# Kernel optimization log

Measured on AMD Instinct MI355X. Metric: run time of the kernel, lower is better.

## Reference

```python
import jax, jax.numpy as jnp
import numpy as np

MIN_HAIRPIN = 4
BIG = 1e30  # stand-in for the numpy reference's 1e18 INF (fp32-safe)


def _dp_single(e_pair, e_unp, allowed):
    """Nussinov min-energy DP for one sequence.
    e_pair: (L,L) f32, e_unp: (L,) f32, allowed: (L,L) bool.
    Returns dp (L,L) and ptr (L,L) backpointers matching the numpy reference:
      0 -> i unpaired, 1 -> j unpaired, 2 -> (i,j) paired, k+3 -> bifurcation at k.
    Vectorised over the antidiagonal (all i for a fixed span s at once).
    """
    L = e_unp.shape[0]
    idx = jnp.arange(L)
    dp0 = jnp.full((L, L), BIG, dtype=e_pair.dtype).at[idx, idx].set(e_unp)
    ptr0 = jnp.full((L, L), -1, dtype=jnp.int32).at[idx, idx].set(0)
    t = jnp.arange(L - 1)  # bifurcation offset k = i + t

    def step(carry, s):
        dp, ptr = carry
        j = idx + s - 1
        valid = j < L
        jc = jnp.minimum(j, L - 1)
        ip1 = jnp.minimum(idx + 1, L - 1)
        jm1 = jnp.maximum(jc - 1, 0)
        opt0 = dp[ip1, jc] + e_unp            # i unpaired
        opt1 = dp[idx, jm1] + e_unp[jc]       # j unpaired
        inner = jnp.where(s >= 3, dp[ip1, jm1], 0.0)
        pair_ok = allowed[idx, jc] & (s - 1 > MIN_HAIRPIN)  # j - i = s - 1
        opt2 = jnp.where(pair_ok, inner + e_pair[idx, jc], BIG)
        k = jnp.minimum(idx[:, None] + t[None, :], L - 1)
        bif = dp[idx[:, None], k] + dp[jnp.minimum(k + 1, L - 1), jc[:, None]]
        bif = jnp.where(t[None, :] < s - 1, bif, BIG)
        cand = jnp.concatenate([opt0[:, None], opt1[:, None], opt2[:, None], bif], axis=1)
        c = jnp.argmin(cand, axis=1)  # first-occurrence argmin == strict-< tie-break
        best = jnp.take_along_axis(cand, c[:, None], axis=1)[:, 0]
        new_ptr = jnp.where(c < 3, c, c + idx).astype(jnp.int32)  # c-3 is offset t -> k+3 = c+i
        dp = dp.at[idx, jc].set(jnp.where(valid, best, dp[idx, jc]))
        ptr = ptr.at[idx, jc].set(jnp.where(valid, new_ptr, ptr[idx, jc]))
        return (dp, ptr), None

    (dp, ptr), _ = jax.lax.scan(step, (dp0, ptr0), jnp.arange(2, L + 1))
    return dp, ptr


def _traceback(ptr):
    """Stack-based traceback of the backpointer matrix. Returns pairs (L,) int32, -1 = unpaired."""
    L = ptr.shape[0]

    def cond(st):
        return st[2] > 0

    def body(st):
        si, sj, sp, res = st
        top = sp - 1
        i, j = si[top], sj[top]
        skip = i >= j
        p = ptr[i, j]
        is0, is1, is2, isk = p == 0, p == 1, p == 2, p >= 3
        k = p - 3
        p1i = jnp.where(is0 | is2, i + 1, i)
        p1j = jnp.where(is1 | is2, j - 1, jnp.where(isk, k, j))
        v1 = (~skip) & jnp.where(is2, i + 1 <= j - 1, True)
        v2 = (~skip) & isk  # bifurcation pushes a second interval (k+1, j)
        res = jnp.where(is2 & (~skip), res.at[i].set(j).at[j].set(i), res)
        si = si.at[top].set(jnp.where(v1, p1i, si[top]))
        sj = sj.at[top].set(jnp.where(v1, p1j, sj[top]))
        slot2 = top + v1.astype(jnp.int32)
        si = si.at[slot2].set(jnp.where(v2, k + 1, si[slot2]))
        sj = sj.at[slot2].set(jnp.where(v2, j, sj[slot2]))
        sp = top + v1.astype(jnp.int32) + v2.astype(jnp.int32)
        return si, sj, sp, res

    si0 = jnp.zeros((L,), jnp.int32)
    sj0 = jnp.zeros((L,), jnp.int32).at[0].set(L - 1)
    res0 = jnp.full((L,), -1, jnp.int32)
    _, _, _, res = jax.lax.while_loop(cond, body, (si0, sj0, jnp.int32(1), res0))
    return res


def _structure_energy(e_pair, e_unp, pairs):
    """E(x,S) = sum_{i unpaired} e_unp[i] + sum_{(i,j) in S, i<j} e_pair[i,j]."""
    L = e_unp.shape[-1]
    clamped = jnp.maximum(pairs, 0)
    unp = jnp.where(pairs < 0, e_unp, 0.0).sum(-1)
    pe = jnp.take_along_axis(e_pair, clamped[..., None], axis=2)[..., 0]
    is_pair = (pairs >= 0) & (jnp.arange(L)[None, :] < clamped)
    return unp + jnp.where(is_pair, pe, 0.0).sum(-1)


def setup_inputs() -> dict:
    key = jax.random.key(0)
    k1, k2, k3 = jax.random.split(key, 3)
    B, L = 32, 384
    e_pair = jax.random.normal(k1, (B, L, L), jnp.float32)
    e_unp = jax.random.normal(k2, (B, L), jnp.float32)
    pair_mask = jax.random.randint(k3, (B, L, L), 0, 2).astype(jnp.bool_)
    return {"e_pair": e_pair, "e_unp": e_unp, "pair_mask": pair_mask}


def reference(e_pair, e_unp, pair_mask):
    dp, ptr = jax.vmap(_dp_single)(e_pair, e_unp, pair_mask)
    pairs = jax.vmap(_traceback)(ptr)  # (B, L) int32, -1 = unpaired
    energy = _structure_energy(e_pair, e_unp, pairs)  # (B,), equals dp[:, 0, -1]
    return pairs, energy
```

## Files before the change

### kernel.cpp

```cpp
#include <hip/hip_runtime.h>

#define LSEQ 384
#define BATCH 32
#define BIGV 1e30f
#define TB_STK 448
#define NN ((size_t)LSEQ * LSEQ)
#define BT 32
#define NT 12
#define PIT 33

__device__ __forceinline__ int detect_mmode_wave(const unsigned char* m0, int lane) {
    unsigned char v = m0[lane & 63];
    unsigned long long big = __ballot(v >= 2);
    unsigned long long off = __ballot((((lane & 63) & 3) != 0) && (v != 0));
    return big ? 2 : (off ? 1 : 0);
}
__device__ __forceinline__ bool mask_read(const void* mask, size_t idx, int mmode) {
    if (mmode == 0) return ((const unsigned int*)mask)[idx] != 0;
    if (mmode == 1) return ((const unsigned char*)mask)[idx] != 0;
    return ((const unsigned short*)mask)[idx] != 0;
}
__device__ __forceinline__ void choice_write(void* mask, size_t idx, int c, int mmode) {
    if (mmode == 0) ((unsigned int*)mask)[idx] = (unsigned int)c;
    else if (mmode == 1) ((unsigned char*)mask)[idx] = (unsigned char)c;
    else ((unsigned short*)mask)[idx] = (unsigned short)c;
}

__device__ __forceinline__ float edge_min32(const float* rowp, const float* colp) {
    float a0 = BIGV, a1 = BIGV, a2 = BIGV, a3 = BIGV;
    #pragma unroll
    for (int kk = 0; kk < 32; kk += 4) {
        float r0 = rowp[kk], r1 = rowp[kk + 1], r2 = rowp[kk + 2], r3 = rowp[kk + 3];
        const float* cb = colp + kk * PIT;
        float c0 = cb[0], c1 = cb[PIT], c2 = cb[2 * PIT], c3 = cb[3 * PIT];
        a0 = fminf(a0, r0 + c0); a1 = fminf(a1, r1 + c1);
        a2 = fminf(a2, r2 + c2); a3 = fminf(a3, r3 + c3);
    }
    return fminf(fminf(a0, a1), fminf(a2, a3));
}

__device__ __forceinline__ void minplus_waves(
    const float* __restrict__ dpG, int I, int J, const int* fm, int nfm,
    int wv, int lane, float part[4][BT][PIT])
{
    const int r0 = (lane >> 3) << 2, c0 = (lane & 7) << 2;
    float r16[16];
    #pragma unroll
    for (int z = 0; z < 16; ++z) r16[z] = BIGV;
    const int mi = wv >> 1, kqB = (wv & 1) * 4;
    if (mi < nfm) {
        const int M = fm[mi];
        #pragma unroll
        for (int q = 0; q < 4; ++q) {
            const int k = M * BT + (kqB + q) * 4;
            float4 a0 = *(const float4*)&dpG[(size_t)(I * BT + r0 + 0) * LSEQ + k];
            float4 a1 = *(const float4*)&dpG[(size_t)(I * BT + r0 + 1) * LSEQ + k];
            float4 a2 = *(const float4*)&dpG[(size_t)(I * BT + r0 + 2) * LSEQ + k];
            float4 a3 = *(const float4*)&dpG[(size_t)(I * BT + r0 + 3) * LSEQ + k];
            float4 b0 = *(const float4*)&dpG[(size_t)(J * BT + c0 + 0) * LSEQ + k];
            float4 b1 = *(const float4*)&dpG[(size_t)(J * BT + c0 + 1) * LSEQ + k];
            float4 b2 = *(const float4*)&dpG[(size_t)(J * BT + c0 + 2) * LSEQ + k];
            float4 b3 = *(const float4*)&dpG[(size_t)(J * BT + c0 + 3) * LSEQ + k];
            #pragma unroll
            for (int ri = 0; ri < 4; ++ri) {
                float4 av = ri == 0 ? a0 : ri == 1 ? a1 : ri == 2 ? a2 : a3;
                #pragma unroll
                for (int ci = 0; ci < 4; ++ci) {
                    float4 bv = ci == 0 ? b0 : ci == 1 ? b1 : ci == 2 ? b2 : b3;
                    float m = fminf(fminf(av.x + bv.x, av.y + bv.y),
                                    fminf(av.z + bv.z, av.w + bv.w));
                    r16[ri * 4 + ci] = fminf(r16[ri * 4 + ci], m);
                }
            }
        }
    }
    #pragma unroll
    for (int ri = 0; ri < 4; ++ri)
        #pragma unroll
        for (int ci = 0; ci < 4; ++ci)
            part[wv][r0 + ri][c0 + ci] = r16[ri * 4 + ci];
}

__device__ __constant__ int c_sb4[12] = {0,0,0,0, 0, 8, 15, 21, 26, 30, 33, 35};

__global__ __launch_bounds__(64) void diag_kernel(
    float* __restrict__ e_pair, const float* __restrict__ e_unp, void* mask)
{
    __shared__ float dT[BT + 1][PIT];
    __shared__ float epm[BT][PIT];
    __shared__ float s_eunp[BT];

    const int bid = blockIdx.x;
    const int b = bid / NT, t = bid % NT;
    const int lane = threadIdx.x;
    float* dpG = e_pair + (size_t)b * NN;
    const size_t mb = (size_t)b * NN;
    const int mmode = detect_mmode_wave((const unsigned char*)mask, lane);

    for (int z = lane; z < (BT + 1) * PIT; z += 64) ((float*)dT)[z] = BIGV;
    __syncthreads();
    if (lane < BT) {
        int i = t * BT + lane;
        float v = e_unp[b * LSEQ + i];
        s_eunp[lane] = v;
        dT[lane][lane] = v;
        dpG[(size_t)i * LSEQ + i] = v;
        if (i > 0) dpG[(size_t)i * LSEQ + i - 1] = v;
    }
    for (int z = lane; z < BT * BT; z += 64) {
        int li = z >> 5, lj = z & 31;
        int i = t * BT + li, j = t * BT + lj;
        bool ok = (lj - li > 4) && mask_read(mask, mb + (size_t)i * LSEQ + j, mmode);
        epm[li][lj] = ok ? dpG[(size_t)i * LSEQ + j] : BIGV;
    }
    __syncthreads();

    const int idx = lane >> 1, h = lane & 1;
    for (int sg = 1; sg < BT; ++sg) {
        const int nc = BT - sg;
        const bool act = idx < nc;
        const int li = idx, lj = idx + sg;
        const int ljc = lj < BT ? lj : BT - 1;
        const int i = t * BT + li, j = t * BT + lj;
        float ev = edge_min32(&dT[li][0], &dT[1][ljc]);
        float e1 = BIGV, opt0 = 0.f, x1 = BIGV, x2 = BIGV;
        if (act) {
            if (h == 0) {
                e1 = ev;
                opt0 = dT[li + 1][lj] + s_eunp[li];
            } else {
                x1 = dT[li][lj - 1] + s_eunp[lj];
                float pe = epm[li][lj];
                if (pe < BIGV) x2 = dT[li + 1][lj - 1] + pe;
            }
        }
        float y1 = __shfl_xor(x1, 1), y2 = __shfl_xor(x2, 1);
        if (act && h == 0) {
            float best = fminf(e1, y2);
            int cch = (best == opt0) ? 0 : (best == y1) ? 1
                     : (best == y2 && y2 < BIGV) ? 2 : 3;
            dT[li][lj] = best;
            dpG[(size_t)i * LSEQ + j] = best;
            if (i > 0) dpG[(size_t)j * LSEQ + i - 1] = best;
            choice_write(mask, mb + (size_t)j * LSEQ + i, cch, mmode);
        }
    }
}

__global__ __launch_bounds__(256) void step_kernel(
    float* __restrict__ e_pair, const float* __restrict__ e_unp,
    void* mask, float* __restrict__ acc, int p)
{
    __shared__ float dTI[BT + 1][PIT], dTJ[BT + 1][PIT];
    __shared__ float cur[BT + 1][PIT];
    __shared__ float epm[BT][PIT];
    __shared__ float part[4][BT][PIT];
    __shared__ float brow[BT], bcol[BT], s_eI[BT], s_eJ[BT];
    __shared__ float bcorn;

    const int b = blockIdx.x % BATCH;
    const int u = blockIdx.x / BATCH;
    const int nswp = NT - p;
    const int tid = threadIdx.x, lane = tid & 63, wv = tid >> 6;
    float* dpG = e_pair + (size_t)b * NN;
    const size_t mb = (size_t)b * NN;

    if (u >= nswp) {
        int e = u - nswp, s2 = p + 1;
        while (s2 < NT && e >= NT - s2) { e -= NT - s2; ++s2; }
        const int I = e, J = I + s2;
        int fm[2]; fm[0] = I + p - 1; int nfm = 1;
        if (J - (p - 1) != fm[0]) fm[nfm++] = J - (p - 1);
        minplus_waves(dpG, I, J, fm, nfm, wv, lane, part);
        __syncthreads();
        float* accT = acc + ((size_t)(b * 36 + c_sb4[s2] + I) << 10);
        const bool first = (p == (s2 + 1) / 2 + 1);
        for (int z = tid; z < BT * BT; z += 256) {
            int li = z >> 5, lj = z & 31;
            float m = fminf(fminf(part[0][li][lj], part[1][li][lj]),
                            fminf(part[2][li][lj], part[3][li][lj]));
            accT[z] = first ? m : fminf(accT[z], m);
        }
        return;
    }

    const int I = u, J = I + p, s = p;
    const int mmode = detect_mmode_wave((const unsigned char*)mask, lane);

    for (int z = tid; z < BT * BT; z += 256) {
        int li = z >> 5, lj = z & 31;
        dTI[li][lj] = (lj >= li) ? dpG[(size_t)(I * BT + li) * LSEQ + I * BT + lj] : BIGV;
        dTJ[li][lj] = (lj >= li) ? dpG[(size_t)(J * BT + li) * LSEQ + J * BT + lj] : BIGV;
    }
    for (int z = tid; z < PIT; z += 256) {
        dTI[BT][z] = BIGV; dTJ[BT][z] = BIGV; cur[BT][z] = BIGV;
    }
    if (tid < BT) {
        brow[tid] = dpG[(size_t)((I + 1) * BT) * LSEQ + J * BT + tid];
        s_eI[tid] = e_unp[b * LSEQ + I * BT + tid];
    } else if (tid < 2 * BT) {
        int q = tid - BT;
        bcol[q] = dpG[(size_t)(I * BT + q) * LSEQ + J * BT - 1];
        s_eJ[q] = e_unp[b * LSEQ + J * BT + q];
    } else if (tid == 2 * BT) {
        bcorn = (s >= 2) ? dpG[(size_t)((I + 1) * BT) * LSEQ + J * BT - 1] : BIGV;
    }
    for (int z = tid; z < BT * BT; z += 256) {
        int li = z >> 5, lj = z & 31;
        int i = I * BT + li, j = J * BT + lj;
        bool ok = (j - i > 4) && mask_read(mask, mb + (size_t)i * LSEQ + j, mmode);
        epm[li][lj] = ok ? dpG[(size_t)i * LSEQ + j] : BIGV;
    }

    int fm[2]; int nfm = 0;
    if (s >= 2) fm[nfm++] = I + 1;
    if (s >= 3) fm[nfm++] = J - 1;
    minplus_waves(dpG, I, J, fm, nfm, wv, lane, part);
    __syncthreads();

    const float* accT = acc + ((size_t)(b * 36 + c_sb4[s] + I) << 10);
    for (int z = tid; z < BT * BT; z += 256) {
        int li = z >> 5, lj = z & 31;
        float m = fminf(fminf(part[0][li][lj], part[1][li][lj]),
                        fminf(part[2][li][lj], part[3][li][lj]));
        if (s >= 4) m = fminf(m, accT[z]);
        cur[li][lj] = m;
    }
    __syncthreads();
    if (wv != 0) return;

    const int idx = lane >> 1, h = lane & 1;
    for (int sg = -(BT - 1); sg <= BT - 1; ++sg) {
        const int asg = sg < 0 ? -sg : sg;
        const int nc = BT - asg;
        const bool act = idx < nc;
        const int li = (sg >= 0) ? idx : idx - sg;
        const int lj = li + sg;
        const int lic = li < BT ? li : BT - 1;
        const int ljc = (lj < BT ? (lj >= 0 ? lj : 0) : BT - 1);
        const int i = I * BT + li, j = J * BT + lj;
        const float* rowp = (h == 0) ? &dTI[lic][0] : &cur[lic][0];
        const float* colp = (h == 0) ? &cur[1][ljc] : &dTJ[1][ljc];
        float ev = edge_min32(rowp, colp);
        float e1 = BIGV, opt0 = 0.f, farv = BIGV;
        float x0 = BIGV, x1 = BIGV, x2 = BIGV;
        if (act) {
            if (h == 0) {
                e1 = fminf(ev, dTI[li][BT - 1] + brow[lj]);
                opt0 = ((li + 1 < BT) ? cur[li + 1][lj] : brow[lj]) + s_eI[li];
                farv = cur[li][lj];
            } else {
                x0 = ev;
                x1 = ((lj >= 1) ? cur[li][lj - 1] : bcol[li]) + s_eJ[lj];
                float pe = epm[li][lj];
                if (pe < BIGV) {
                    float inner = (li + 1 < BT)
                        ? ((lj >= 1) ? cur[li + 1][lj - 1] : bcol[li + 1])
                        : ((lj >= 1) ? brow[lj - 1] : bcorn);
                    x2 = inner + pe;
                }
            }
        }
        float y0 = __shfl_xor(x0, 1), y1 = __shfl_xor(x1, 1), y2 = __shfl_xor(x2, 1);
        if (act && h == 0) {
            float best = fminf(fminf(fminf(e1, y0), farv), y2);
            int cch = (best == opt0) ? 0 : (best == y1) ? 1
                     : (best == y2 && y2 < BIGV) ? 2 : 3;
            cur[li][lj] = best;
            dpG[(size_t)i * LSEQ + j] = best;
            if (i > 0) dpG[(size_t)j * LSEQ + i - 1] = best;
            choice_write(mask, mb + (size_t)j * LSEQ + i, cch, mmode);
        }
    }
}

__global__ __launch_bounds__(512) void tb_kernel(
    const float* __restrict__ e_pair, const void* mask, float* __restrict__ out)
{
    const int b = blockIdx.x;
    const int tid = threadIdx.x;
    const int lane = tid & 63, wv = tid >> 6;
    const float* dp = e_pair + (size_t)b * NN;
    const size_t mb = (size_t)b * NN;
    const int mmode = detect_mmode_wave((const unsigned char*)mask, lane);

    __shared__ __align__(16) unsigned char ch[LSEQ * LSEQ];
    __shared__ short res[LSEQ];
    __shared__ int st[TB_STK];

    if (mmode == 1) {
        const uint4* src = (const uint4*)((const unsigned char*)mask + mb);
        for (int z = tid; z < (int)(NN / 16); z += 512) ((uint4*)ch)[z] = src[z];
    } else if (mmode == 2) {
        const uint4* src = (const uint4*)((const unsigned char*)mask + mb * 2);
        for (int z = tid; z < (int)(NN / 8); z += 512) {
            uint4 v = src[z];
            unsigned int lo = (v.x & 0xFFu) | (((v.x >> 16) & 0xFFu) << 8)
                            | ((v.y & 0xFFu) << 16) | (((v.y >> 16) & 0xFFu) << 24);
            unsigned int hi = (v.z & 0xFFu) | (((v.z >> 16) & 0xFFu) << 8)
                            | ((v.w & 0xFFu) << 16) | (((v.w >> 16) & 0xFFu) << 24);
            ((unsigned int*)ch)[z * 2] = lo;
            ((unsigned int*)ch)[z * 2 + 1] = hi;
        }
    } else {
        const uint4* src = (const uint4*)((const unsigned char*)mask + mb * 4);
        for (int z = tid; z < (int)(NN / 4); z += 512) {
            uint4 v = src[z];
            ((unsigned int*)ch)[z] = (v.x & 0xFFu) | ((v.y & 0xFFu) << 8)
                                   | ((v.z & 0xFFu) << 16) | ((v.w & 0xFFu) << 24);
        }
    }
    for (int l = tid; l < LSEQ; l += 512) res[l] = -1;
    __syncthreads();
    if (wv != 0) return;

    int sp = 0;
    int ci = 0, cj = LSEQ - 1;
    int have = 1;
    for (int iter = 0; iter < 8192; ++iter) {
        if (!have) {
            if (sp == 0) break;
            --sp;
            int pk = st[sp];
            ci = pk >> 16; cj = pk & 0xFFFF;
        }
        have = 0;
        if (ci >= cj) continue;
        int c = ch[(size_t)cj * LSEQ + ci];
        if (c == 0) { ++ci; have = 1; }
        else if (c == 1) { --cj; have = 1; }
        else if (c == 2) {
            res[ci] = (short)cj; res[cj] = (short)ci;
            if (ci + 1 <= cj - 1) { ++ci; --cj; have = 1; }
        } else {
            const int d = cj - ci;
            const float* rowi = dp + (size_t)ci * LSEQ;
            const float* mrow = dp + (size_t)cj * LSEQ;
            float bv = BIGV; int bt = d;
            for (int t = lane; t < d; t += 64) {
                float cc = rowi[ci + t] + mrow[ci + t];
                if (cc < bv || (cc == bv && t < bt)) { bv = cc; bt = t; }
            }
            for (int m = 32; m > 0; m >>= 1) {
                float ov = __shfl_xor(bv, m, 64);
                int   ot = __shfl_xor(bt, m, 64);
                if (ov < bv || (ov == bv && ot < bt)) { bv = ov; bt = ot; }
            }
            int k = ci + bt;
            if (sp < TB_STK - 1) { st[sp] = ((k + 1) << 16) | cj; ++sp; }
            cj = k; have = 1;
        }
    }

    for (int l = lane; l < LSEQ; l += 64)
        out[b * LSEQ + l] = (float)res[l];
    if (lane == 0)
        out[BATCH * LSEQ + b] = dp[LSEQ - 1];
}

extern "C" void kernel_launch(void* const* d_in, const int* in_sizes, int n_in,
                              void* d_out, int out_size, void* d_ws, size_t ws_size,
                              hipStream_t stream) {
    float* e_pair = (float*)d_in[0];
    const float* e_unp = (const float*)d_in[1];
    void* mask = d_in[2];
    float* acc = (float*)d_ws;
    (void)ws_size;

    static const int updC[12] = {0, 0, 0, 8, 13, 15, 14, 10, 6, 3, 1, 0};

    diag_kernel<<<BATCH * NT, 64, 0, stream>>>(e_pair, e_unp, mask);
    for (int p = 1; p < NT; ++p)
        step_kernel<<<BATCH * (NT - p + updC[p]), 256, 0, stream>>>(
            e_pair, e_unp, mask, acc, p);
    tb_kernel<<<BATCH, 512, 0, stream>>>(e_pair, mask, (float*)d_out);
}
```

Measured before the change: 775.6 us.

## Fuse diagonal and wavefront step kernels into one cooperative persistent kernel

Replaces the diag kernel and the eleven per-wavefront step kernel launches with a single cooperative kernel. It loops over tiles with a grid-stride loop and uses grid.sync() between wavefront phases. This removes per-launch overhead and the gaps between kernel boundaries. In exchange, the diagonal phase now runs in 256-thread blocks with only one wave active, the grid is capped by occupancy, and every phase pays a grid-wide barrier.

```diff
diff --git a/kernel.cpp b/kernel.cpp
--- a/kernel.cpp
+++ b/kernel.cpp
@@ -1,4 +1,5 @@
 #include <hip/hip_runtime.h>
+#include <hip/hip_cooperative_groups.h>
 
 #define LSEQ 384
 #define BATCH 32
@@ -8,6 +9,8 @@
 #define BT 32
 #define NT 12
 #define PIT 33
+
+namespace cg = cooperative_groups;
 
 __device__ __forceinline__ int detect_mmode_wave(const unsigned char* m0, int lane) {
     unsigned char v = m0[lane & 63];
@@ -82,75 +85,14 @@
 }
 
 __device__ __constant__ int c_sb4[12] = {0,0,0,0, 0, 8, 15, 21, 26, 30, 33, 35};
-
-__global__ __launch_bounds__(64) void diag_kernel(
-    float* __restrict__ e_pair, const float* __restrict__ e_unp, void* mask)
+__device__ __constant__ int c_updC[12] = {0, 0, 0, 8, 13, 15, 14, 10, 6, 3, 1, 0};
+
+__global__ __launch_bounds__(256, 3) void dp_coop(
+    float* __restrict__ e_pair, const float* __restrict__ e_unp,
+    void* mask, float* __restrict__ acc)
 {
-    __shared__ float dT[BT + 1][PIT];
-    __shared__ float epm[BT][PIT];
-    __shared__ float s_eunp[BT];
-
-    const int bid = blockIdx.x;
-    const int b = bid / NT, t = bid % NT;
-    const int lane = threadIdx.x;
-    float* dpG = e_pair + (size_t)b * NN;
-    const size_t mb = (size_t)b * NN;
-    const int mmode = detect_mmode_wave((const unsigned char*)mask, lane);
-
-    for (int z = lane; z < (BT + 1) * PIT; z += 64) ((float*)dT)[z] = BIGV;
-    __syncthreads();
-    if (lane < BT) {
-        int i = t * BT + lane;
-        float v = e_unp[b * LSEQ + i];
-        s_eunp[lane] = v;
-        dT[lane][lane] = v;
-        dpG[(size_t)i * LSEQ + i] = v;
-        if (i > 0) dpG[(size_t)i * LSEQ + i - 1] = v;
-    }
-    for (int z = lane; z < BT * BT; z += 64) {
-        int li = z >> 5, lj = z & 31;
-        int i = t * BT + li, j = t * BT + lj;
-        bool ok = (lj - li > 4) && mask_read(mask, mb + (size_t)i * LSEQ + j, mmode);
-        epm[li][lj] = ok ? dpG[(size_t)i * LSEQ + j] : BIGV;
-    }
-    __syncthreads();
-
-    const int idx = lane >> 1, h = lane & 1;
-    for (int sg = 1; sg < BT; ++sg) {
-        const int nc = BT - sg;
-        const bool act = idx < nc;
-        const int li = idx, lj = idx + sg;
-        const int ljc = lj < BT ? lj : BT - 1;
-        const int i = t * BT + li, j = t * BT + lj;
-        float ev = edge_min32(&dT[li][0], &dT[1][ljc]);
-        float e1 = BIGV, opt0 = 0.f, x1 = BIGV, x2 = BIGV;
-        if (act) {
-            if (h == 0) {
-                e1 = ev;
-                opt0 = dT[li + 1][lj] + s_eunp[li];
-            } else {
-                x1 = dT[li][lj - 1] + s_eunp[lj];
-                float pe = epm[li][lj];
-                if (pe < BIGV) x2 = dT[li + 1][lj - 1] + pe;
-            }
-        }
-        float y1 = __shfl_xor(x1, 1), y2 = __shfl_xor(x2, 1);
-        if (act && h == 0) {
-            float best = fminf(e1, y2);
-            int cch = (best == opt0) ? 0 : (best == y1) ? 1
-                     : (best == y2 && y2 < BIGV) ? 2 : 3;
-            dT[li][lj] = best;
-            dpG[(size_t)i * LSEQ + j] = best;
-            if (i > 0) dpG[(size_t)j * LSEQ + i - 1] = best;
-            choice_write(mask, mb + (size_t)j * LSEQ + i, cch, mmode);
-        }
-    }
-}
-
-__global__ __launch_bounds__(256) void step_kernel(
-    float* __restrict__ e_pair, const float* __restrict__ e_unp,
-    void* mask, float* __restrict__ acc, int p)
-{
+    cg::grid_group grid = cg::this_grid();
+
     __shared__ float dTI[BT + 1][PIT], dTJ[BT + 1][PIT];
     __shared__ float cur[BT + 1][PIT];
     __shared__ float epm[BT][PIT];
@@ -158,119 +100,187 @@
     __shared__ float brow[BT], bcol[BT], s_eI[BT], s_eJ[BT];
     __shared__ float bcorn;
 
-    const int b = blockIdx.x % BATCH;
-    const int u = blockIdx.x / BATCH;
-    const int nswp = NT - p;
     const int tid = threadIdx.x, lane = tid & 63, wv = tid >> 6;
-    float* dpG = e_pair + (size_t)b * NN;
-    const size_t mb = (size_t)b * NN;
-
-    if (u >= nswp) {
-        int e = u - nswp, s2 = p + 1;
-        while (s2 < NT && e >= NT - s2) { e -= NT - s2; ++s2; }
-        const int I = e, J = I + s2;
-        int fm[2]; fm[0] = I + p - 1; int nfm = 1;
-        if (J - (p - 1) != fm[0]) fm[nfm++] = J - (p - 1);
-        minplus_waves(dpG, I, J, fm, nfm, wv, lane, part);
+    const int mmode = detect_mmode_wave((const unsigned char*)mask, lane);
+
+    for (int it = blockIdx.x; it < BATCH * NT; it += gridDim.x) {
+        const int b = it % BATCH, t = it / BATCH;
+        float* dpG = e_pair + (size_t)b * NN;
+        const size_t mb = (size_t)b * NN;
+
+        for (int z = tid; z < (BT + 1) * PIT; z += 256) ((float*)dTI)[z] = BIGV;
         __syncthreads();
-        float* accT = acc + ((size_t)(b * 36 + c_sb4[s2] + I) << 10);
-        const bool first = (p == (s2 + 1) / 2 + 1);
+        if (tid < BT) {
+            int i = t * BT + tid;
+            float v = e_unp[b * LSEQ + i];
+            s_eI[tid] = v;
+            dTI[tid][tid] = v;
+            dpG[(size_t)i * LSEQ + i] = v;
+            if (i > 0) dpG[(size_t)i * LSEQ + i - 1] = v;
+        }
         for (int z = tid; z < BT * BT; z += 256) {
             int li = z >> 5, lj = z & 31;
-            float m = fminf(fminf(part[0][li][lj], part[1][li][lj]),
-                            fminf(part[2][li][lj], part[3][li][lj]));
-            accT[z] = first ? m : fminf(accT[z], m);
-        }
-        return;
-    }
-
-    const int I = u, J = I + p, s = p;
-    const int mmode = detect_mmode_wave((const unsigned char*)mask, lane);
-
-    for (int z = tid; z < BT * BT; z += 256) {
-        int li = z >> 5, lj = z & 31;
-        dTI[li][lj] = (lj >= li) ? dpG[(size_t)(I * BT + li) * LSEQ + I * BT + lj] : BIGV;
-        dTJ[li][lj] = (lj >= li) ? dpG[(size_t)(J * BT + li) * LSEQ + J * BT + lj] : BIGV;
-    }
-    for (int z = tid; z < PIT; z += 256) {
-        dTI[BT][z] = BIGV; dTJ[BT][z] = BIGV; cur[BT][z] = BIGV;
-    }
-    if (tid < BT) {
-        brow[tid] = dpG[(size_t)((I + 1) * BT) * LSEQ + J * BT + tid];
-        s_eI[tid] = e_unp[b * LSEQ + I * BT + tid];
-    } else if (tid < 2 * BT) {
-        int q = tid - BT;
-        bcol[q] = dpG[(size_t)(I * BT + q) * LSEQ + J * BT - 1];
-        s_eJ[q] = e_unp[b * LSEQ + J * BT + q];
-    } else if (tid == 2 * BT) {
-        bcorn = (s >= 2) ? dpG[(size_t)((I + 1) * BT) * LSEQ + J * BT - 1] : BIGV;
-    }
-    for (int z = tid; z < BT * BT; z += 256) {
-        int li = z >> 5, lj = z & 31;
-        int i = I * BT + li, j = J * BT + lj;
-        bool ok = (j - i > 4) && mask_read(mask, mb + (size_t)i * LSEQ + j, mmode);
-        epm[li][lj] = ok ? dpG[(size_t)i * LSEQ + j] : BIGV;
-    }
-
-    int fm[2]; int nfm = 0;
-    if (s >= 2) fm[nfm++] = I + 1;
-    if (s >= 3) fm[nfm++] = J - 1;
-    minplus_waves(dpG, I, J, fm, nfm, wv, lane, part);
-    __syncthreads();
-
-    const float* accT = acc + ((size_t)(b * 36 + c_sb4[s] + I) << 10);
-    for (int z = tid; z < BT * BT; z += 256) {
-        int li = z >> 5, lj = z & 31;
-        float m = fminf(fminf(part[0][li][lj], part[1][li][lj]),
-                        fminf(part[2][li][lj], part[3][li][lj]));
-        if (s >= 4) m = fminf(m, accT[z]);
-        cur[li][lj] = m;
-    }
-    __syncthreads();
-    if (wv != 0) return;
-
-    const int idx = lane >> 1, h = lane & 1;
-    for (int sg = -(BT - 1); sg <= BT - 1; ++sg) {
-        const int asg = sg < 0 ? -sg : sg;
-        const int nc = BT - asg;
-        const bool act = idx < nc;
-        const int li = (sg >= 0) ? idx : idx - sg;
-        const int lj = li + sg;
-        const int lic = li < BT ? li : BT - 1;
-        const int ljc = (lj < BT ? (lj >= 0 ? lj : 0) : BT - 1);
-        const int i = I * BT + li, j = J * BT + lj;
-        const float* rowp = (h == 0) ? &dTI[lic][0] : &cur[lic][0];
-        const float* colp = (h == 0) ? &cur[1][ljc] : &dTJ[1][ljc];
-        float ev = edge_min32(rowp, colp);
-        float e1 = BIGV, opt0 = 0.f, farv = BIGV;
-        float x0 = BIGV, x1 = BIGV, x2 = BIGV;
-        if (act) {
-            if (h == 0) {
-                e1 = fminf(ev, dTI[li][BT - 1] + brow[lj]);
-                opt0 = ((li + 1 < BT) ? cur[li + 1][lj] : brow[lj]) + s_eI[li];
-                farv = cur[li][lj];
-            } else {
-                x0 = ev;
-                x1 = ((lj >= 1) ? cur[li][lj - 1] : bcol[li]) + s_eJ[lj];
-                float pe = epm[li][lj];
-                if (pe < BIGV) {
-                    float inner = (li + 1 < BT)
-                        ? ((lj >= 1) ? cur[li + 1][lj - 1] : bcol[li + 1])
-                        : ((lj >= 1) ? brow[lj - 1] : bcorn);
-                    x2 = inner + pe;
-                }
-            }
-        }
-        float y0 = __shfl_xor(x0, 1), y1 = __shfl_xor(x1, 1), y2 = __shfl_xor(x2, 1);
-        if (act && h == 0) {
-            float best = fminf(fminf(fminf(e1, y0), farv), y2);
-            int cch = (best == opt0) ? 0 : (best == y1) ? 1
-                     : (best == y2 && y2 < BIGV) ? 2 : 3;
-            cur[li][lj] = best;
-            dpG[(size_t)i * LSEQ + j] = best;
-            if (i > 0) dpG[(size_t)j * LSEQ + i - 1] = best;
-            choice_write(mask, mb + (size_t)j * LSEQ + i, cch, mmode);
-        }
+            int i = t * BT + li, j = t * BT + lj;
+            bool ok = (lj - li > 4) && mask_read(mask, mb + (size_t)i * LSEQ + j, mmode);
+            epm[li][lj] = ok ? dpG[(size_t)i * LSEQ + j] : BIGV;
+        }
+        __syncthreads();
+        if (wv == 0) {
+            const int idx = lane >> 1, h = lane & 1;
+            for (int sg = 1; sg < BT; ++sg) {
+                const int nc = BT - sg;
+                const bool act = idx < nc;
+                const int li = idx, lj = idx + sg;
+                const int ljc = lj < BT ? lj : BT - 1;
+                const int i = t * BT + li, j = t * BT + lj;
+                float ev = edge_min32(&dTI[li][0], &dTI[1][ljc]);
+                float e1 = BIGV, opt0 = 0.f, x1 = BIGV, x2 = BIGV;
+                if (act) {
+                    if (h == 0) {
+                        e1 = ev;
+                        opt0 = dTI[li + 1][lj] + s_eI[li];
+                    } else {
+                        x1 = dTI[li][lj - 1] + s_eI[lj];
+                        float pe = epm[li][lj];
+                        if (pe < BIGV) x2 = dTI[li + 1][lj - 1] + pe;
+                    }
+                }
+                float y1 = __shfl_xor(x1, 1), y2 = __shfl_xor(x2, 1);
+                if (act && h == 0) {
+                    float best = fminf(e1, y2);
+                    int cch = (best == opt0) ? 0 : (best == y1) ? 1
+                             : (best == y2 && y2 < BIGV) ? 2 : 3;
+                    dTI[li][lj] = best;
+                    dpG[(size_t)i * LSEQ + j] = best;
+                    if (i > 0) dpG[(size_t)j * LSEQ + i - 1] = best;
+                    choice_write(mask, mb + (size_t)j * LSEQ + i, cch, mmode);
+                }
+            }
+        }
+        __syncthreads();
+    }
+    grid.sync();
+
+    for (int p = 1; p < NT; ++p) {
+        const int nswp = NT - p;
+        const int tot = BATCH * (nswp + c_updC[p]);
+        for (int it = blockIdx.x; it < tot; it += gridDim.x) {
+            const int b = it % BATCH;
+            const int u = it / BATCH;
+            float* dpG = e_pair + (size_t)b * NN;
+            const size_t mb = (size_t)b * NN;
+
+            if (u >= nswp) {
+                int e = u - nswp, s2 = p + 1;
+                while (s2 < NT && e >= NT - s2) { e -= NT - s2; ++s2; }
+                const int I = e, J = I + s2;
+                int fm[2]; fm[0] = I + p - 1; int nfm = 1;
+                if (J - (p - 1) != fm[0]) fm[nfm++] = J - (p - 1);
+                minplus_waves(dpG, I, J, fm, nfm, wv, lane, part);
+                __syncthreads();
+                float* accT = acc + ((size_t)(b * 36 + c_sb4[s2] + I) << 10);
+                const bool first = (p == (s2 + 1) / 2 + 1);
+                for (int z = tid; z < BT * BT; z += 256) {
+                    int li = z >> 5, lj = z & 31;
+                    float m = fminf(fminf(part[0][li][lj], part[1][li][lj]),
+                                    fminf(part[2][li][lj], part[3][li][lj]));
+                    accT[z] = first ? m : fminf(accT[z], m);
+                }
+                __syncthreads();
+                continue;
+            }
+
+            const int I = u, J = I + p, s = p;
+
+            for (int z = tid; z < BT * BT; z += 256) {
+                int li = z >> 5, lj = z & 31;
+                dTI[li][lj] = (lj >= li) ? dpG[(size_t)(I * BT + li) * LSEQ + I * BT + lj] : BIGV;
+                dTJ[li][lj] = (lj >= li) ? dpG[(size_t)(J * BT + li) * LSEQ + J * BT + lj] : BIGV;
+            }
+            for (int z = tid; z < PIT; z += 256) {
+                dTI[BT][z] = BIGV; dTJ[BT][z] = BIGV; cur[BT][z] = BIGV;
+            }
+            if (tid < BT) {
+                brow[tid] = dpG[(size_t)((I + 1) * BT) * LSEQ + J * BT + tid];
+                s_eI[tid] = e_unp[b * LSEQ + I * BT + tid];
+            } else if (tid < 2 * BT) {
+                int q = tid - BT;
+                bcol[q] = dpG[(size_t)(I * BT + q) * LSEQ + J * BT - 1];
+                s_eJ[q] = e_unp[b * LSEQ + J * BT + q];
+            } else if (tid == 2 * BT) {
+                bcorn = (s >= 2) ? dpG[(size_t)((I + 1) * BT) * LSEQ + J * BT - 1] : BIGV;
+            }
+            for (int z = tid; z < BT * BT; z += 256) {
+                int li = z >> 5, lj = z & 31;
+                int i = I * BT + li, j = J * BT + lj;
+                bool ok = (j - i > 4) && mask_read(mask, mb + (size_t)i * LSEQ + j, mmode);
+                epm[li][lj] = ok ? dpG[(size_t)i * LSEQ + j] : BIGV;
+            }
+
+            int fm[2]; int nfm = 0;
+            if (s >= 2) fm[nfm++] = I + 1;
+            if (s >= 3) fm[nfm++] = J - 1;
+            minplus_waves(dpG, I, J, fm, nfm, wv, lane, part);
+            __syncthreads();
+
+            const float* accT = acc + ((size_t)(b * 36 + c_sb4[s] + I) << 10);
+            for (int z = tid; z < BT * BT; z += 256) {
+                int li = z >> 5, lj = z & 31;
+                float m = fminf(fminf(part[0][li][lj], part[1][li][lj]),
+                                fminf(part[2][li][lj], part[3][li][lj]));
+                if (s >= 4) m = fminf(m, accT[z]);
+                cur[li][lj] = m;
+            }
+            __syncthreads();
+
+            if (wv == 0) {
+                const int idx = lane >> 1, h = lane & 1;
+                for (int sg = -(BT - 1); sg <= BT - 1; ++sg) {
+                    const int asg = sg < 0 ? -sg : sg;
+                    const int nc = BT - asg;
+                    const bool act = idx < nc;
+                    const int li = (sg >= 0) ? idx : idx - sg;
+                    const int lj = li + sg;
+                    const int lic = li < BT ? li : BT - 1;
+                    const int ljc = (lj < BT ? (lj >= 0 ? lj : 0) : BT - 1);
+                    const int i = I * BT + li, j = J * BT + lj;
+                    const float* rowp = (h == 0) ? &dTI[lic][0] : &cur[lic][0];
+                    const float* colp = (h == 0) ? &cur[1][ljc] : &dTJ[1][ljc];
+                    float ev = edge_min32(rowp, colp);
+                    float e1 = BIGV, opt0 = 0.f, farv = BIGV;
+                    float x0 = BIGV, x1 = BIGV, x2 = BIGV;
+                    if (act) {
+                        if (h == 0) {
+                            e1 = fminf(ev, dTI[li][BT - 1] + brow[lj]);
+                            opt0 = ((li + 1 < BT) ? cur[li + 1][lj] : brow[lj]) + s_eI[li];
+                            farv = cur[li][lj];
+                        } else {
+                            x0 = ev;
+                            x1 = ((lj >= 1) ? cur[li][lj - 1] : bcol[li]) + s_eJ[lj];
+                            float pe = epm[li][lj];
+                            if (pe < BIGV) {
+                                float inner = (li + 1 < BT)
+                                    ? ((lj >= 1) ? cur[li + 1][lj - 1] : bcol[li + 1])
+                                    : ((lj >= 1) ? brow[lj - 1] : bcorn);
+                                x2 = inner + pe;
+                            }
+                        }
+                    }
+                    float y0 = __shfl_xor(x0, 1), y1 = __shfl_xor(x1, 1), y2 = __shfl_xor(x2, 1);
+                    if (act && h == 0) {
+                        float best = fminf(fminf(fminf(e1, y0), farv), y2);
+                        int cch = (best == opt0) ? 0 : (best == y1) ? 1
+                                 : (best == y2 && y2 < BIGV) ? 2 : 3;
+                        cur[li][lj] = best;
+                        dpG[(size_t)i * LSEQ + j] = best;
+                        if (i > 0) dpG[(size_t)j * LSEQ + i - 1] = best;
+                        choice_write(mask, mb + (size_t)j * LSEQ + i, cch, mmode);
+                    }
+                }
+            }
+            __syncthreads();
+        }
+        grid.sync();
     }
 }
 
@@ -367,11 +377,15 @@
     float* acc = (float*)d_ws;
     (void)ws_size;
 
-    static const int updC[12] = {0, 0, 0, 8, 13, 15, 14, 10, 6, 3, 1, 0};
-
-    diag_kernel<<<BATCH * NT, 64, 0, stream>>>(e_pair, e_unp, mask);
-    for (int p = 1; p < NT; ++p)
-        step_kernel<<<BATCH * (NT - p + updC[p]), 256, 0, stream>>>(
-            e_pair, e_unp, mask, acc, p);
+    int mpc = 0;
+    if (hipOccupancyMaxActiveBlocksPerMultiprocessor(&mpc, dp_coop, 256, 0)
+            != hipSuccess || mpc < 1)
+        mpc = 2;
+    int grid = mpc * 256;
+    if (grid > 704) grid = 704;
+
+    void* args[] = { (void*)&e_pair, (void*)&e_unp, (void*)&mask, (void*)&acc };
+    hipLaunchCooperativeKernel((void*)dp_coop, dim3(grid), dim3(256),
+                               args, 0, stream);
     tb_kernel<<<BATCH, 512, 0, stream>>>(e_pair, mask, (float*)d_out);
 }
```

After: 1.229 ms. 1.58x slower.

## Fuse last three DP wavefront steps and traceback into one per-sequence tail kernel

Applied to the files above, without the earlier changes.

Replaces the final three step_kernel launches (p=9..11) and the separate traceback kernel with one tail_kernel per sequence. It runs the remaining min-plus and diagonal tile tasks serially inside one block, writes choice codes straight into a packed triangular shared-memory array, then runs the traceback. This removes several launch and sync boundaries on the narrow end of the wavefront, where little parallelism is left. The cost is that the final tiles run on only one block per sequence (32 blocks total), with a large shared-memory footprint that limits occupancy.

```diff
diff --git a/kernel.cpp b/kernel.cpp
--- a/kernel.cpp
+++ b/kernel.cpp
@@ -8,6 +8,7 @@
 #define BT 32
 #define NT 12
 #define PIT 33
+#define TRI_SZ 73536
 
 __device__ __forceinline__ int detect_mmode_wave(const unsigned char* m0, int lane) {
     unsigned char v = m0[lane & 63];
@@ -274,88 +275,188 @@
     }
 }
 
-__global__ __launch_bounds__(512) void tb_kernel(
-    const float* __restrict__ e_pair, const void* mask, float* __restrict__ out)
+__global__ __launch_bounds__(256) void tail_kernel(
+    float* __restrict__ e_pair, const float* __restrict__ e_unp,
+    void* mask, float* __restrict__ acc, float* __restrict__ out)
 {
+    __shared__ unsigned char ch[TRI_SZ];
+    __shared__ float dTI[BT + 1][PIT], dTJ[BT + 1][PIT];
+    __shared__ float cur[BT + 1][PIT];
+    __shared__ float epm[BT][PIT];
+    __shared__ float part[4][BT][PIT];
+    __shared__ float brow[BT], bcol[BT], s_eI[BT], s_eJ[BT];
+    __shared__ float bcorn;
+    __shared__ short res[LSEQ];
+    __shared__ int st[TB_STK];
+
     const int b = blockIdx.x;
-    const int tid = threadIdx.x;
-    const int lane = tid & 63, wv = tid >> 6;
-    const float* dp = e_pair + (size_t)b * NN;
+    const int tid = threadIdx.x, lane = tid & 63, wv = tid >> 6;
+    float* dpG = e_pair + (size_t)b * NN;
     const size_t mb = (size_t)b * NN;
     const int mmode = detect_mmode_wave((const unsigned char*)mask, lane);
 
-    __shared__ __align__(16) unsigned char ch[LSEQ * LSEQ];
-    __shared__ short res[LSEQ];
-    __shared__ int st[TB_STK];
-
-    if (mmode == 1) {
-        const uint4* src = (const uint4*)((const unsigned char*)mask + mb);
-        for (int z = tid; z < (int)(NN / 16); z += 512) ((uint4*)ch)[z] = src[z];
-    } else if (mmode == 2) {
-        const uint4* src = (const uint4*)((const unsigned char*)mask + mb * 2);
-        for (int z = tid; z < (int)(NN / 8); z += 512) {
-            uint4 v = src[z];
-            unsigned int lo = (v.x & 0xFFu) | (((v.x >> 16) & 0xFFu) << 8)
-                            | ((v.y & 0xFFu) << 16) | (((v.y >> 16) & 0xFFu) << 24);
-            unsigned int hi = (v.z & 0xFFu) | (((v.z >> 16) & 0xFFu) << 8)
-                            | ((v.w & 0xFFu) << 16) | (((v.w >> 16) & 0xFFu) << 24);
-            ((unsigned int*)ch)[z * 2] = lo;
-            ((unsigned int*)ch)[z * 2 + 1] = hi;
-        }
-    } else {
-        const uint4* src = (const uint4*)((const unsigned char*)mask + mb * 4);
-        for (int z = tid; z < (int)(NN / 4); z += 512) {
-            uint4 v = src[z];
-            ((unsigned int*)ch)[z] = (v.x & 0xFFu) | ((v.y & 0xFFu) << 8)
-                                   | ((v.z & 0xFFu) << 16) | ((v.w & 0xFFu) << 24);
-        }
-    }
-    for (int l = tid; l < LSEQ; l += 512) res[l] = -1;
+    {
+        const unsigned char* mbase = (const unsigned char*)mask;
+        const int esz = (mmode == 0) ? 4 : (mmode == 1) ? 1 : 2;
+        for (int j = wv; j < LSEQ; j += 4) {
+            const size_t go = (mb + (size_t)j * LSEQ) * esz;
+            const size_t lo = (size_t)j * (j - 1) / 2;
+            for (int i = lane; i < j; i += 64)
+                ch[lo + i] = mbase[go + (size_t)i * esz];
+        }
+    }
+    for (int l = tid; l < LSEQ; l += 256) res[l] = -1;
+    for (int z = tid; z < PIT; z += 256) {
+        dTI[BT][z] = BIGV; dTJ[BT][z] = BIGV; cur[BT][z] = BIGV;
+    }
     __syncthreads();
-    if (wv != 0) return;
-
-    int sp = 0;
-    int ci = 0, cj = LSEQ - 1;
-    int have = 1;
-    for (int iter = 0; iter < 8192; ++iter) {
-        if (!have) {
-            if (sp == 0) break;
-            --sp;
-            int pk = st[sp];
-            ci = pk >> 16; cj = pk & 0xFFFF;
-        }
-        have = 0;
-        if (ci >= cj) continue;
-        int c = ch[(size_t)cj * LSEQ + ci];
-        if (c == 0) { ++ci; have = 1; }
-        else if (c == 1) { --cj; have = 1; }
-        else if (c == 2) {
-            res[ci] = (short)cj; res[cj] = (short)ci;
-            if (ci + 1 <= cj - 1) { ++ci; --cj; have = 1; }
-        } else {
-            const int d = cj - ci;
-            const float* rowi = dp + (size_t)ci * LSEQ;
-            const float* mrow = dp + (size_t)cj * LSEQ;
-            float bv = BIGV; int bt = d;
-            for (int t = lane; t < d; t += 64) {
-                float cc = rowi[ci + t] + mrow[ci + t];
-                if (cc < bv || (cc == bv && t < bt)) { bv = cc; bt = t; }
-            }
-            for (int m = 32; m > 0; m >>= 1) {
-                float ov = __shfl_xor(bv, m, 64);
-                int   ot = __shfl_xor(bt, m, 64);
-                if (ov < bv || (ov == bv && ot < bt)) { bv = ov; bt = ot; }
-            }
-            int k = ci + bt;
-            if (sp < TB_STK - 1) { st[sp] = ((k + 1) << 16) | cj; ++sp; }
-            cj = k; have = 1;
-        }
-    }
-
-    for (int l = lane; l < LSEQ; l += 64)
-        out[b * LSEQ + l] = (float)res[l];
-    if (lane == 0)
-        out[BATCH * LSEQ + b] = dp[LSEQ - 1];
+
+    static const int tasks[10][5] = {
+        {0, 0, 10, 8, 2}, {0, 1, 11, 9, 3}, {0, 0, 11, 8, 3},
+        {1, 0, 9, 0, 0}, {1, 1, 10, 0, 0}, {1, 2, 11, 0, 0},
+        {0, 0, 11, 9, 2},
+        {1, 0, 10, 0, 0}, {1, 1, 11, 0, 0},
+        {1, 0, 11, 0, 0} };
+
+    for (int tk = 0; tk < 10; ++tk) {
+        const int I = tasks[tk][1], J = tasks[tk][2], s = J - I;
+        if (tasks[tk][0] == 0) {
+            int fm[2] = { tasks[tk][3], tasks[tk][4] };
+            minplus_waves(dpG, I, J, fm, 2, wv, lane, part);
+            __syncthreads();
+            float* accT = acc + ((size_t)(b * 36 + c_sb4[s] + I) << 10);
+            for (int z = tid; z < BT * BT; z += 256) {
+                int li = z >> 5, lj = z & 31;
+                float m = fminf(fminf(part[0][li][lj], part[1][li][lj]),
+                                fminf(part[2][li][lj], part[3][li][lj]));
+                accT[z] = fminf(accT[z], m);
+            }
+            __syncthreads();
+            continue;
+        }
+        for (int z = tid; z < BT * BT; z += 256) {
+            int li = z >> 5, lj = z & 31;
+            dTI[li][lj] = (lj >= li) ? dpG[(size_t)(I * BT + li) * LSEQ + I * BT + lj] : BIGV;
+            dTJ[li][lj] = (lj >= li) ? dpG[(size_t)(J * BT + li) * LSEQ + J * BT + lj] : BIGV;
+        }
+        if (tid < BT) {
+            brow[tid] = dpG[(size_t)((I + 1) * BT) * LSEQ + J * BT + tid];
+            s_eI[tid] = e_unp[b * LSEQ + I * BT + tid];
+        } else if (tid < 2 * BT) {
+            int q = tid - BT;
+            bcol[q] = dpG[(size_t)(I * BT + q) * LSEQ + J * BT - 1];
+            s_eJ[q] = e_unp[b * LSEQ + J * BT + q];
+        } else if (tid == 2 * BT) {
+            bcorn = dpG[(size_t)((I + 1) * BT) * LSEQ + J * BT - 1];
+        }
+        for (int z = tid; z < BT * BT; z += 256) {
+            int li = z >> 5, lj = z & 31;
+            int i = I * BT + li, j = J * BT + lj;
+            bool ok = (j - i > 4) && mask_read(mask, mb + (size_t)i * LSEQ + j, mmode);
+            epm[li][lj] = ok ? dpG[(size_t)i * LSEQ + j] : BIGV;
+        }
+        int fm[2] = { I + 1, J - 1 };
+        minplus_waves(dpG, I, J, fm, 2, wv, lane, part);
+        __syncthreads();
+        const float* accT = acc + ((size_t)(b * 36 + c_sb4[s] + I) << 10);
+        for (int z = tid; z < BT * BT; z += 256) {
+            int li = z >> 5, lj = z & 31;
+            float m = fminf(fminf(part[0][li][lj], part[1][li][lj]),
+                            fminf(part[2][li][lj], part[3][li][lj]));
+            cur[li][lj] = fminf(m, accT[z]);
+        }
+        __syncthreads();
+        if (wv == 0) {
+            const int idx = lane >> 1, h = lane & 1;
+            for (int sg = -(BT - 1); sg <= BT - 1; ++sg) {
+                const int asg = sg < 0 ? -sg : sg;
+                const int nc = BT - asg;
+                const bool act = idx < nc;
+                const int li = (sg >= 0) ? idx : idx - sg;
+                const int lj = li + sg;
+                const int lic = li < BT ? li : BT - 1;
+                const int ljc = (lj < BT ? (lj >= 0 ? lj : 0) : BT - 1);
+                const int i = I * BT + li, j = J * BT + lj;
+                const float* rowp = (h == 0) ? &dTI[lic][0] : &cur[lic][0];
+                const float* colp = (h == 0) ? &cur[1][ljc] : &dTJ[1][ljc];
+                float ev = edge_min32(rowp, colp);
+                float e1 = BIGV, opt0 = 0.f, farv = BIGV;
+                float x0 = BIGV, x1 = BIGV, x2 = BIGV;
+                if (act) {
+                    if (h == 0) {
+                        e1 = fminf(ev, dTI[li][BT - 1] + brow[lj]);
+                        opt0 = ((li + 1 < BT) ? cur[li + 1][lj] : brow[lj]) + s_eI[li];
+                        farv = cur[li][lj];
+                    } else {
+                        x0 = ev;
+                        x1 = ((lj >= 1) ? cur[li][lj - 1] : bcol[li]) + s_eJ[lj];
+                        float pe = epm[li][lj];
+                        if (pe < BIGV) {
+                            float inner = (li + 1 < BT)
+                                ? ((lj >= 1) ? cur[li + 1][lj - 1] : bcol[li + 1])
+                                : ((lj >= 1) ? brow[lj - 1] : bcorn);
+                            x2 = inner + pe;
+                        }
+                    }
+                }
+                float y0 = __shfl_xor(x0, 1), y1 = __shfl_xor(x1, 1), y2 = __shfl_xor(x2, 1);
+                if (act && h == 0) {
+                    float best = fminf(fminf(fminf(e1, y0), farv), y2);
+                    int cch = (best == opt0) ? 0 : (best == y1) ? 1
+                             : (best == y2 && y2 < BIGV) ? 2 : 3;
+                    cur[li][lj] = best;
+                    dpG[(size_t)i * LSEQ + j] = best;
+                    if (i > 0) dpG[(size_t)j * LSEQ + i - 1] = best;
+                    ch[(size_t)j * (j - 1) / 2 + i] = (unsigned char)cch;
+                }
+            }
+        }
+        __syncthreads();
+    }
+
+    if (wv == 0) {
+        int sp = 0;
+        int ci = 0, cj = LSEQ - 1;
+        int have = 1;
+        for (int iter = 0; iter < 8192; ++iter) {
+            if (!have) {
+                if (sp == 0) break;
+                --sp;
+                int pk = st[sp];
+                ci = pk >> 16; cj = pk & 0xFFFF;
+            }
+            have = 0;
+            if (ci >= cj) continue;
+            int c = ch[(size_t)(cj * (cj - 1) >> 1) + ci];
+            if (c == 0) { ++ci; have = 1; }
+            else if (c == 1) { --cj; have = 1; }
+            else if (c == 2) {
+                res[ci] = (short)cj; res[cj] = (short)ci;
+                if (ci + 1 <= cj - 1) { ++ci; --cj; have = 1; }
+            } else {
+                const int d = cj - ci;
+                const float* rowi = dpG + (size_t)ci * LSEQ;
+                const float* mrow = dpG + (size_t)cj * LSEQ;
+                float bv = BIGV; int bt = d;
+                for (int t = lane; t < d; t += 64) {
+                    float cc = rowi[ci + t] + mrow[ci + t];
+                    if (cc < bv || (cc == bv && t < bt)) { bv = cc; bt = t; }
+                }
+                for (int m = 32; m > 0; m >>= 1) {
+                    float ov = __shfl_xor(bv, m, 64);
+                    int   ot = __shfl_xor(bt, m, 64);
+                    if (ov < bv || (ov == bv && ot < bt)) { bv = ov; bt = ot; }
+                }
+                int k = ci + bt;
+                if (sp < TB_STK - 1) { st[sp] = ((k + 1) << 16) | cj; ++sp; }
+                cj = k; have = 1;
+            }
+        }
+        for (int l = lane; l < LSEQ; l += 64)
+            out[b * LSEQ + l] = (float)res[l];
+        if (lane == 0)
+            out[BATCH * LSEQ + b] = dpG[LSEQ - 1];
+    }
 }
 
 extern "C" void kernel_launch(void* const* d_in, const int* in_sizes, int n_in,
@@ -367,11 +468,11 @@
     float* acc = (float*)d_ws;
     (void)ws_size;
 
-    static const int updC[12] = {0, 0, 0, 8, 13, 15, 14, 10, 6, 3, 1, 0};
+    static const int updC[9] = {0, 0, 0, 8, 13, 15, 14, 10, 6};
 
     diag_kernel<<<BATCH * NT, 64, 0, stream>>>(e_pair, e_unp, mask);
-    for (int p = 1; p < NT; ++p)
+    for (int p = 1; p <= 8; ++p)
         step_kernel<<<BATCH * (NT - p + updC[p]), 256, 0, stream>>>(
             e_pair, e_unp, mask, acc, p);
-    tb_kernel<<<BATCH, 512, 0, stream>>>(e_pair, mask, (float*)d_out);
-}
+    tail_kernel<<<BATCH, 256, 0, stream>>>(e_pair, e_unp, mask, acc, (float*)d_out);
+}
```

Result: slower. 1.029 ms (+32.6%).
